# Optimization experiments

Hardware: AMD Instinct MI355X
Metric: run time of the kernel (lower is better)

## Reference

```python
import jax, jax.numpy as jnp
import numpy as np

RADIUS = 0.4
NSAMPLE = 32


def setup_inputs() -> dict:
    key = jax.random.key(0)
    ks = jax.random.split(key, 6)
    B, N, C = 2, 16384, 64
    xyz = jax.random.normal(ks[0], (B, N, 3), jnp.float32)
    features = jax.random.normal(ks[1], (B, C, N), jnp.float32)

    def w(k, i, o):
        return jax.random.normal(k, (i, o), jnp.float32) * (1.0 / np.sqrt(i))

    W1 = w(ks[2], C + 3, 64)
    W2 = w(ks[3], 64, 64)
    W3 = w(ks[4], 64, 128)
    return {
        "xyz": xyz, "features": features,
        "W1": W1, "b1": jnp.zeros((64,), jnp.float32),
        "W2": W2, "b2": jnp.zeros((64,), jnp.float32),
        "W3": W3, "b3": jnp.zeros((128,), jnp.float32),
        "npoint": 4096,
    }


def ball_query(xyz, new_xyz, radius, nsample):
    """xyz [B,N,3], new_xyz [B,S,3] -> neighbor idx [B,S,nsample] int32.
    Replicates pointnet2 ball_query: first `nsample` points (in index order)
    within `radius` of each centroid; empty slots filled with the first hit
    (0 if no point is in range)."""
    N = xyz.shape[1]
    # squared distances [B,S,N] via ||a||^2 + ||b||^2 - 2 a.b
    d2 = (jnp.sum(new_xyz * new_xyz, -1)[:, :, None]
          + jnp.sum(xyz * xyz, -1)[:, None, :]
          - 2.0 * jnp.einsum('bsc,bnc->bsn', new_xyz, xyz))
    cand = jnp.where(d2 < radius * radius,
                     jnp.arange(N, dtype=jnp.int32), jnp.int32(N))
    neg_topk, _ = jax.lax.top_k(-cand, nsample)  # nsample smallest indices
    idx = -neg_topk
    first = idx[..., :1]
    idx = jnp.where(idx == N, first, idx)  # pad with first valid neighbor
    idx = jnp.where(idx == N, 0, idx)      # no neighbor at all -> 0
    return idx


def reference(xyz, features, W1, b1, W2, b2, W3, b3, npoint):
    B = xyz.shape[0]
    # sample_method=None, keep_first_half=False -> idx = arange(npoint)
    new_xyz = xyz[:, :npoint]                        # [B,S,3]
    idx = ball_query(jax.lax.stop_gradient(xyz),
                     jax.lax.stop_gradient(new_xyz), RADIUS, NSAMPLE)
    # group: gather neighbors, re-center xyz, concat features (use_xyz=True)
    grouped_xyz = jax.vmap(lambda p, i: p[i])(xyz, idx) - new_xyz[:, :, None]  # [B,S,K,3]
    feats_nc = features.transpose(0, 2, 1)           # [B,N,C]
    grouped_f = jax.vmap(lambda f, i: f[i])(feats_nc, idx)  # [B,S,K,C]
    g = jnp.concatenate([grouped_xyz, grouped_f], axis=-1)  # [B,S,K,3+C]
    # shared MLP (1x1 convs + ReLU)
    h = jax.nn.relu(jnp.einsum('bskc,cd->bskd', g, W1) + b1)
    h = jax.nn.relu(jnp.einsum('bskc,cd->bskd', h, W2) + b2)
    h = jax.nn.relu(jnp.einsum('bskc,cd->bskd', h, W3) + b3)
    new_features = jnp.max(h, axis=2).transpose(0, 2, 1)    # [B,128,S]
    samp_idx = jnp.tile(jnp.arange(npoint, dtype=jnp.int32), (B, 1))
    return new_xyz, new_features, samp_idx
```

## Files before the change

kernel.cpp:

```cpp
#include <hip/hip_runtime.h>

#define BB 2
#define NN 16384
#define CC 64
#define SS 4096
#define KK 32
#define R2 0.16f

#define GD   32
#define GC   (GD * GD * GD)
#define CAP  1024
#define CAPL (CAP / 64)

typedef __bf16 bf16x8 __attribute__((ext_vector_type(8)));
typedef float  f32x4  __attribute__((ext_vector_type(4)));

#define MFMA(a, b, c) __builtin_amdgcn_mfma_f32_16x16x32_bf16((a), (b), (c), 0, 0, 0)

static __device__ __forceinline__ ushort f2bf(float f) {
    __bf16 h = (__bf16)f;
    return *(ushort*)&h;
}

static __device__ __forceinline__ int cellc(float x) {
    int i = (int)floorf(x * 2.5f + 16.0f);
    return i < 0 ? 0 : (i > GD - 1 ? GD - 1 : i);
}

#define WS_PTS4   0
#define WS_FEAT   524288
#define WS_W1T    4718592
#define WS_W2T    4730880
#define WS_W3T    4739072
#define WS_SPTS   4755456
#define WS_SSID   5279744
#define WS_CNT    5410816
#define WS_OFF    5672960

#define T_PTS   (BB * NN)
#define T_W1    (T_PTS + 64 * 96)
#define T_W2    (T_W1 + 64 * 64)
#define T_W3    (T_W2 + 128 * 64)
#define T_NXYZ  (T_W3 + BB * SS * 3)
#define T_SIDX  (T_NXYZ + BB * SS)
#define T_ALL   (T_SIDX + BB * NN * 8)

__global__ __launch_bounds__(256) void prep_kernel(
        const float* __restrict__ xyz, const float* __restrict__ feat,
        const float* __restrict__ W1, const float* __restrict__ W2,
        const float* __restrict__ W3,
        float4* __restrict__ pts4, ushort* __restrict__ feat_nc,
        ushort* __restrict__ W1t, ushort* __restrict__ W2t,
        ushort* __restrict__ W3t,
        float* __restrict__ out_xyz, float* __restrict__ out_sidx,
        uint* __restrict__ counts) {
    const int t = blockIdx.x * 256 + threadIdx.x;
    if (t < T_PTS) {
        const float* p = xyz + (size_t)t * 3;
        const float x = p[0], y = p[1], z = p[2];
        pts4[t] = make_float4(x, y, z, x * x + y * y + z * z);
        const int cell = (((cellc(z) << 5) + cellc(y)) << 5) + cellc(x);
        atomicAdd(&counts[(t >> 14) * GC + cell], 1u);
    } else if (t < T_W1) {
        const int i = t - T_PTS;
        const int n = i / 96, k = i - n * 96;
        float v = 0.0f;
        if (k < 64) v = W1[(3 + k) * 64 + n];
        else if (k < 67) v = W1[(k - 64) * 64 + n];
        W1t[n * 96 + k] = f2bf(v);
    } else if (t < T_W2) {
        const int i = t - T_W1;
        const int n = i >> 6, k = i & 63;
        W2t[n * 64 + k] = f2bf(W2[k * 64 + n]);
    } else if (t < T_W3) {
        const int i = t - T_W2;
        const int n = i >> 6, k = i & 63;
        W3t[n * 64 + k] = f2bf(W3[k * 128 + n]);
    } else if (t < T_NXYZ) {
        const int i = t - T_W3;
        const int b = i / (SS * 3), j = i - b * (SS * 3);
        out_xyz[i] = xyz[(size_t)b * NN * 3 + j];
    } else if (t < T_SIDX) {
        const int i = t - T_NXYZ;
        out_sidx[i] = (float)(i & (SS - 1));
    } else if (t < T_ALL) {
        const int j = t - T_SIDX;
        const int nl = j >> 3, c8 = j & 7;
        const int b = nl >> 14, n = nl & (NN - 1);
        const float* fb = feat + (size_t)b * CC * NN + n;
        uint u[4];
        #pragma unroll
        for (int q = 0; q < 4; ++q) {
            const float f0 = fb[(size_t)(c8 * 8 + 2 * q) * NN];
            const float f1 = fb[(size_t)(c8 * 8 + 2 * q + 1) * NN];
            u[q] = (uint)f2bf(f0) | ((uint)f2bf(f1) << 16);
        }
        *(uint4*)(feat_nc + (size_t)nl * 64 + c8 * 8) = make_uint4(u[0], u[1], u[2], u[3]);
    }
}

__global__ __launch_bounds__(1024) void scan_kernel(uint* __restrict__ counts,
                                                    uint* __restrict__ offs) {
    __shared__ int lds[1024];
    const int b = blockIdx.x, t = threadIdx.x;
    uint* cnts = counts + (size_t)b * GC;
    uint* off  = offs + (size_t)b * 32772;
    int sum = 0;
    #pragma unroll
    for (int j = 0; j < 8; ++j) {
        const uint4 v = *((const uint4*)cnts + t * 8 + j);
        sum += (int)(v.x + v.y + v.z + v.w);
    }
    lds[t] = sum;
    __syncthreads();
    for (int d = 1; d < 1024; d <<= 1) {
        const int add = (t >= d) ? lds[t - d] : 0;
        __syncthreads();
        lds[t] += add;
        __syncthreads();
    }
    int run = lds[t] - sum;
    #pragma unroll 4
    for (int j = 0; j < 32; ++j) {
        const int ci = t * 32 + j;
        const uint cv = cnts[ci];
        off[ci] = (uint)run;
        cnts[ci] = (uint)run;
        run += (int)cv;
    }
    if (t == 1023) off[GC] = (uint)run;
}

__global__ __launch_bounds__(256) void scatter_kernel(
        const float4* __restrict__ pts4, uint* __restrict__ counts,
        float4* __restrict__ spts, int* __restrict__ ssid) {
    const int t = blockIdx.x * 256 + threadIdx.x;
    const int b = t >> 14;
    const float4 p = pts4[t];
    const int cell = (((cellc(p.z) << 5) + cellc(p.y)) << 5) + cellc(p.x);
    const uint pos = atomicAdd(&counts[(size_t)b * GC + cell], 1u);
    spts[(size_t)b * NN + pos] = p;
    ssid[(size_t)b * NN + pos] = t & (NN - 1);
}

__global__ __launch_bounds__(256, 2) void fused_kernel(
        const float4* __restrict__ pts4, const ushort* __restrict__ feat_nc,
        const float4* __restrict__ spts, const int* __restrict__ ssid,
        const uint* __restrict__ offs,
        const ushort* __restrict__ W1t, const ushort* __restrict__ W2t,
        const ushort* __restrict__ W3t,
        const float* __restrict__ b1, const float* __restrict__ b2,
        const float* __restrict__ b3, float* __restrict__ out_feat) {
    const int w = threadIdx.x >> 6, lane = threadIdx.x & 63;
    const int quad = lane >> 4, mrow = lane & 15;
    const int m = lane & 31, half = lane >> 5;

    __shared__ __align__(16) ushort ldsA[4][32 * 104];
    __shared__ float stage[128][5];
    ushort* gbuf = ldsA[w];
    int* hit = (int*)gbuf;

    const int xcd = blockIdx.x & 7;
    const int slot = blockIdx.x >> 3;
    const int b = xcd >> 2;
    const int s0 = ((xcd & 3) * 256 + slot) * 4;
    const int s = s0 + w;

    const float4* pb = pts4 + (size_t)b * NN;
    const ushort* fbase = feat_nc + (size_t)b * NN * 64;
    const unsigned long long ltmask = (1ull << lane) - 1ull;

    {
        const float4 c = pb[s];
        const int cx = cellc(c.x), cy = cellc(c.y), cz = cellc(c.z);
        const int x0 = cx - 1 < 0 ? 0 : cx - 1;
        const int x1 = cx + 1 > GD - 1 ? GD - 1 : cx + 1;
        const uint* off = offs + (size_t)b * 32772;
        const float4* sp = spts + (size_t)b * NN;
        const int* sidp = ssid + (size_t)b * NN;
        int cnt = 0;
        #pragma unroll
        for (int e = 0; e < 9; ++e) {
            const int z = cz + e / 3 - 1, y = cy + e % 3 - 1;
            const bool ok = (z >= 0) && (z < GD) && (y >= 0) && (y < GD);
            const int cb = ((z << 5) + y) << 5;
            const int rs = ok ? (int)off[cb + x0] : 0;
            const int re = ok ? (int)off[cb + x1 + 1] : 0;
            for (int i0 = rs; i0 < re; i0 += 64) {
                const int iw = i0 + lane;
                const int ii = iw < re - 1 ? iw : re - 1;
                const bool act = iw < re;
                const float4 p = sp[ii];
                const int id = sidp[ii];
                const float d = c.w + p.w - 2.0f * (c.x * p.x + c.y * p.y + c.z * p.z);
                const bool h = act && (d < R2);
                const unsigned long long mk = __ballot(h);
                if (mk != 0ull) {
                    if (h) {
                        const int pp = cnt + __popcll(mk & ltmask);
                        if (pp < CAP) hit[pp] = id;
                    }
                    cnt += __popcll(mk);
                }
            }
        }
        if (cnt > KK) {
            const int stored = cnt < CAP ? cnt : CAP;
            int v[CAPL];
            #pragma unroll
            for (int j = 0; j < CAPL; ++j) {
                const int q = j * 64 + lane;
                v[j] = (q < stored) ? hit[q] : 0x7fffffff;
            }
            int lo = 0, hi = NN - 1;
            while (lo < hi) {
                const int mid = (lo + hi) >> 1;
                int cle = 0;
                #pragma unroll
                for (int j = 0; j < CAPL; ++j) cle += (v[j] <= mid) ? 1 : 0;
                #pragma unroll
                for (int o = 1; o < 64; o <<= 1) cle += __shfl_xor(cle, o);
                if (cle >= KK) hi = mid; else lo = mid + 1;
            }
            int pos = 0;
            #pragma unroll
            for (int j = 0; j < CAPL; ++j) {
                const bool sel = v[j] <= lo;
                const unsigned long long mk = __ballot(sel);
                if (sel) hit[pos + __popcll(mk & ltmask)] = v[j];
                pos += __popcll(mk);
            }
        } else if (lane < KK) {
            const int vv = (cnt == 0) ? 0 : ((lane < cnt) ? hit[lane] : hit[0]);
            hit[lane] = vv;
        }
    }

    {
        const int sid = hit[m];
        const ushort* src = fbase + (size_t)sid * 64 + half * 32;
        ushort* dst = gbuf + m * 104 + half * 32;
        uint4 rows[4];
        #pragma unroll
        for (int i = 0; i < 4; ++i) rows[i] = *(const uint4*)(src + i * 8);
        const float4 p = pb[sid];
        const float4 cc = pb[s];
        #pragma unroll
        for (int i = 0; i < 4; ++i) *(uint4*)(dst + i * 8) = rows[i];
        if (half == 0) {
            bf16x8 rel = {(__bf16)(p.x - cc.x), (__bf16)(p.y - cc.y),
                          (__bf16)(p.z - cc.z), (__bf16)0.f,
                          (__bf16)0.f, (__bf16)0.f, (__bf16)0.f, (__bf16)0.f};
            *(bf16x8*)(gbuf + m * 104 + 64) = rel;
            *(uint4*)(gbuf + m * 104 + 88) = make_uint4(0, 0, 0, 0);
        } else {
            *(uint4*)(gbuf + m * 104 + 72) = make_uint4(0, 0, 0, 0);
            *(uint4*)(gbuf + m * 104 + 80) = make_uint4(0, 0, 0, 0);
        }
    }

    {
        f32x4 acc[2][4];
        #pragma unroll
        for (int nt = 0; nt < 4; ++nt) {
            const float bv = b1[nt * 16 + mrow];
            acc[0][nt] = (f32x4){bv, bv, bv, bv};
            acc[1][nt] = acc[0][nt];
        }
        #pragma unroll
        for (int ks = 0; ks < 3; ++ks) {
            const bf16x8 a0 = *(const bf16x8*)(gbuf + mrow * 104 + ks * 32 + quad * 8);
            const bf16x8 a1 = *(const bf16x8*)(gbuf + (16 + mrow) * 104 + ks * 32 + quad * 8);
            #pragma unroll
            for (int nt = 0; nt < 4; ++nt) {
                const bf16x8 wf = *(const bf16x8*)(W1t + (nt * 16 + mrow) * 96 + ks * 32 + quad * 8);
                acc[0][nt] = MFMA(a0, wf, acc[0][nt]);
                acc[1][nt] = MFMA(a1, wf, acc[1][nt]);
            }
        }
        #pragma unroll
        for (int mt = 0; mt < 2; ++mt)
            #pragma unroll
            for (int nt = 0; nt < 4; ++nt)
                #pragma unroll
                for (int r = 0; r < 4; ++r)
                    gbuf[(mt * 16 + quad * 4 + r) * 104 + nt * 16 + mrow] =
                        f2bf(fmaxf(acc[mt][nt][r], 0.0f));
    }

    {
        f32x4 acc[2][4];
        #pragma unroll
        for (int nt = 0; nt < 4; ++nt) {
            const float bv = b2[nt * 16 + mrow];
            acc[0][nt] = (f32x4){bv, bv, bv, bv};
            acc[1][nt] = acc[0][nt];
        }
        #pragma unroll
        for (int ks = 0; ks < 2; ++ks) {
            const bf16x8 a0 = *(const bf16x8*)(gbuf + mrow * 104 + ks * 32 + quad * 8);
            const bf16x8 a1 = *(const bf16x8*)(gbuf + (16 + mrow) * 104 + ks * 32 + quad * 8);
            #pragma unroll
            for (int nt = 0; nt < 4; ++nt) {
                const bf16x8 wf = *(const bf16x8*)(W2t + (nt * 16 + mrow) * 64 + ks * 32 + quad * 8);
                acc[0][nt] = MFMA(a0, wf, acc[0][nt]);
                acc[1][nt] = MFMA(a1, wf, acc[1][nt]);
            }
        }
        #pragma unroll
        for (int mt = 0; mt < 2; ++mt)
            #pragma unroll
            for (int nt = 0; nt < 4; ++nt)
                #pragma unroll
                for (int r = 0; r < 4; ++r)
                    gbuf[(mt * 16 + quad * 4 + r) * 104 + nt * 16 + mrow] =
                        f2bf(fmaxf(acc[mt][nt][r], 0.0f));
    }

    #pragma unroll
    for (int nh = 0; nh < 2; ++nh) {
        f32x4 acc[2][4];
        #pragma unroll
        for (int ntl = 0; ntl < 4; ++ntl) {
            const float bv = b3[(nh * 4 + ntl) * 16 + mrow];
            acc[0][ntl] = (f32x4){bv, bv, bv, bv};
            acc[1][ntl] = acc[0][ntl];
        }
        #pragma unroll
        for (int ks = 0; ks < 2; ++ks) {
            const bf16x8 a0 = *(const bf16x8*)(gbuf + mrow * 104 + ks * 32 + quad * 8);
            const bf16x8 a1 = *(const bf16x8*)(gbuf + (16 + mrow) * 104 + ks * 32 + quad * 8);
            #pragma unroll
            for (int ntl = 0; ntl < 4; ++ntl) {
                const bf16x8 wf = *(const bf16x8*)(
                    W3t + ((nh * 4 + ntl) * 16 + mrow) * 64 + ks * 32 + quad * 8);
                acc[0][ntl] = MFMA(a0, wf, acc[0][ntl]);
                acc[1][ntl] = MFMA(a1, wf, acc[1][ntl]);
            }
        }
        #pragma unroll
        for (int ntl = 0; ntl < 4; ++ntl) {
            const f32x4 v0 = acc[0][ntl], v1 = acc[1][ntl];
            float mx = fmaxf(fmaxf(v0[0], v0[1]), fmaxf(v0[2], v0[3]));
            mx = fmaxf(mx, fmaxf(fmaxf(v1[0], v1[1]), fmaxf(v1[2], v1[3])));
            mx = fmaxf(mx, __shfl_xor(mx, 16));
            mx = fmaxf(mx, __shfl_xor(mx, 32));
            mx = fmaxf(mx, 0.0f);
            if (quad == 0) stage[(nh * 4 + ntl) * 16 + mrow][w] = mx;
        }
    }
    __syncthreads();

    {
        const int ch = threadIdx.x & 127;
        const int hf = threadIdx.x >> 7;
        float* dst = out_feat + ((size_t)b * 128 + ch) * SS + s0 + hf * 2;
        *(float2*)dst = make_float2(stage[ch][hf * 2], stage[ch][hf * 2 + 1]);
    }
}

extern "C" void kernel_launch(void* const* d_in, const int* in_sizes, int n_in,
                              void* d_out, int out_size, void* d_ws, size_t ws_size,
                              hipStream_t stream) {
    const float* xyz  = (const float*)d_in[0];
    const float* feat = (const float*)d_in[1];
    const float* W1   = (const float*)d_in[2];
    const float* b1   = (const float*)d_in[3];
    const float* W2   = (const float*)d_in[4];
    const float* b2   = (const float*)d_in[5];
    const float* W3   = (const float*)d_in[6];
    const float* b3   = (const float*)d_in[7];

    float* out      = (float*)d_out;
    float* out_xyz  = out;
    float* out_feat = out + (size_t)BB * SS * 3;
    float* out_sidx = out_feat + (size_t)BB * 128 * SS;

    char* ws = (char*)d_ws;
    float4* pts4    = (float4*)(ws + WS_PTS4);
    ushort* feat_nc = (ushort*)(ws + WS_FEAT);
    ushort* W1t     = (ushort*)(ws + WS_W1T);
    ushort* W2t     = (ushort*)(ws + WS_W2T);
    ushort* W3t     = (ushort*)(ws + WS_W3T);
    float4* spts    = (float4*)(ws + WS_SPTS);
    int*    ssid    = (int*)(ws + WS_SSID);
    uint*   counts  = (uint*)(ws + WS_CNT);
    uint*   offs    = (uint*)(ws + WS_OFF);

    hipMemsetAsync(counts, 0, (size_t)BB * GC * 4, stream);
    prep_kernel<<<(T_ALL + 255) / 256, 256, 0, stream>>>(
        xyz, feat, W1, W2, W3, pts4, feat_nc, W1t, W2t, W3t, out_xyz, out_sidx,
        counts);
    scan_kernel<<<BB, 1024, 0, stream>>>(counts, offs);
    scatter_kernel<<<BB * NN / 256, 256, 0, stream>>>(pts4, counts, spts, ssid);
    fused_kernel<<<BB * SS / 4, 256, 0, stream>>>(pts4, feat_nc, spts, ssid, offs,
                                                  W1t, W2t, W3t, b1, b2, b3,
                                                  out_feat);
}
```

Measured before the change: 168.3 us.

## Shrink grid, fuse histogram/scan/scatter into one LDS bin kernel, flatten neighbor scan

The uniform grid shrinks from 32^3 to 24^3 cells so its histogram fits in LDS. The memset, scan and scatter launches are replaced by one per-batch kernel that builds the histogram with LDS atomics, does a wave-shuffle scan and scatters points. Prep now writes only per-point cell ids. In the fused kernel, the nine candidate ranges are merged into one flat loop so partial wave iterations are shared across ranges, and the hit cap is halved with ballot-based counting in the selection step. The bin kernel runs on only two blocks, which may serialize, and the smaller cap could overflow in dense regions.

```diff
diff --git a/kernel.cpp b/kernel.cpp
--- a/kernel.cpp
+++ b/kernel.cpp
@@ -7,9 +7,10 @@
 #define KK 32
 #define R2 0.16f
 
-#define GD   32
+#define GD   24
 #define GC   (GD * GD * GD)
-#define CAP  1024
+#define GCP  (GC + 4)
+#define CAP  512
 #define CAPL (CAP / 64)
 
 typedef __bf16 bf16x8 __attribute__((ext_vector_type(8)));
@@ -23,7 +24,7 @@
 }
 
 static __device__ __forceinline__ int cellc(float x) {
-    int i = (int)floorf(x * 2.5f + 16.0f);
+    int i = (int)floorf(x * 2.5f + 12.0f);
     return i < 0 ? 0 : (i > GD - 1 ? GD - 1 : i);
 }
 
@@ -34,8 +35,8 @@
 #define WS_W3T    4739072
 #define WS_SPTS   4755456
 #define WS_SSID   5279744
-#define WS_CNT    5410816
-#define WS_OFF    5672960
+#define WS_CELLS  5410816
+#define WS_OFF    5476352
 
 #define T_PTS   (BB * NN)
 #define T_W1    (T_PTS + 64 * 96)
@@ -53,14 +54,13 @@
         ushort* __restrict__ W1t, ushort* __restrict__ W2t,
         ushort* __restrict__ W3t,
         float* __restrict__ out_xyz, float* __restrict__ out_sidx,
-        uint* __restrict__ counts) {
+        ushort* __restrict__ cells) {
     const int t = blockIdx.x * 256 + threadIdx.x;
     if (t < T_PTS) {
         const float* p = xyz + (size_t)t * 3;
         const float x = p[0], y = p[1], z = p[2];
         pts4[t] = make_float4(x, y, z, x * x + y * y + z * z);
-        const int cell = (((cellc(z) << 5) + cellc(y)) << 5) + cellc(x);
-        atomicAdd(&counts[(t >> 14) * GC + cell], 1u);
+        cells[t] = (ushort)((cellc(z) * GD + cellc(y)) * GD + cellc(x));
     } else if (t < T_W1) {
         const int i = t - T_PTS;
         const int n = i / 96, k = i - n * 96;
@@ -99,48 +99,60 @@
     }
 }
 
-__global__ __launch_bounds__(1024) void scan_kernel(uint* __restrict__ counts,
-                                                    uint* __restrict__ offs) {
-    __shared__ int lds[1024];
+#define CH 14
+__global__ __launch_bounds__(1024) void bin_kernel(
+        const float4* __restrict__ pts4, const ushort* __restrict__ cells,
+        float4* __restrict__ spts, int* __restrict__ ssid,
+        uint* __restrict__ offs) {
+    __shared__ uint hist[GC];
+    __shared__ uint wsum[17];
     const int b = blockIdx.x, t = threadIdx.x;
-    uint* cnts = counts + (size_t)b * GC;
-    uint* off  = offs + (size_t)b * 32772;
-    int sum = 0;
+    const ushort* cb = cells + (size_t)b * NN;
+
+    for (int i = t; i < GC; i += 1024) hist[i] = 0u;
+    __syncthreads();
+    for (int i = t; i < NN; i += 1024) atomicAdd(&hist[cb[i]], 1u);
+    __syncthreads();
+
+    uint c[CH];
+    uint s = 0;
     #pragma unroll
-    for (int j = 0; j < 8; ++j) {
-        const uint4 v = *((const uint4*)cnts + t * 8 + j);
-        sum += (int)(v.x + v.y + v.z + v.w);
-    }
-    lds[t] = sum;
-    __syncthreads();
-    for (int d = 1; d < 1024; d <<= 1) {
-        const int add = (t >= d) ? lds[t - d] : 0;
-        __syncthreads();
-        lds[t] += add;
-        __syncthreads();
-    }
-    int run = lds[t] - sum;
-    #pragma unroll 4
-    for (int j = 0; j < 32; ++j) {
-        const int ci = t * 32 + j;
-        const uint cv = cnts[ci];
-        off[ci] = (uint)run;
-        cnts[ci] = (uint)run;
-        run += (int)cv;
-    }
-    if (t == 1023) off[GC] = (uint)run;
-}
-
-__global__ __launch_bounds__(256) void scatter_kernel(
-        const float4* __restrict__ pts4, uint* __restrict__ counts,
-        float4* __restrict__ spts, int* __restrict__ ssid) {
-    const int t = blockIdx.x * 256 + threadIdx.x;
-    const int b = t >> 14;
-    const float4 p = pts4[t];
-    const int cell = (((cellc(p.z) << 5) + cellc(p.y)) << 5) + cellc(p.x);
-    const uint pos = atomicAdd(&counts[(size_t)b * GC + cell], 1u);
-    spts[(size_t)b * NN + pos] = p;
-    ssid[(size_t)b * NN + pos] = t & (NN - 1);
+    for (int j = 0; j < CH; ++j) {
+        const int ci = t * CH + j;
+        c[j] = (ci < GC) ? hist[ci] : 0u;
+        s += c[j];
+    }
+    const int lane = t & 63, wid = t >> 6;
+    uint inc = s;
+    #pragma unroll
+    for (int o = 1; o < 64; o <<= 1) {
+        const uint u = __shfl_up(inc, o);
+        inc += (lane >= o) ? u : 0u;
+    }
+    if (lane == 63) wsum[wid] = inc;
+    __syncthreads();
+    if (t == 0) {
+        uint r = 0;
+        #pragma unroll
+        for (int k = 0; k < 16; ++k) { const uint v2 = wsum[k]; wsum[k] = r; r += v2; }
+    }
+    __syncthreads();
+    uint run = wsum[wid] + inc - s;
+    uint* offb = offs + (size_t)b * GCP;
+    #pragma unroll
+    for (int j = 0; j < CH; ++j) {
+        const int ci = t * CH + j;
+        if (ci < GC) { offb[ci] = run; hist[ci] = run; run += c[j]; }
+    }
+    if (t == 1023) offb[GC] = NN;
+    __syncthreads();
+
+    for (int i = t; i < NN; i += 1024) {
+        const int cell = cb[i];
+        const uint pos = atomicAdd(&hist[cell], 1u);
+        spts[(size_t)b * NN + pos] = pts4[(size_t)b * NN + i];
+        ssid[(size_t)b * NN + pos] = i;
+    }
 }
 
 __global__ __launch_bounds__(256, 2) void fused_kernel(
@@ -175,60 +187,73 @@
         const int cx = cellc(c.x), cy = cellc(c.y), cz = cellc(c.z);
         const int x0 = cx - 1 < 0 ? 0 : cx - 1;
         const int x1 = cx + 1 > GD - 1 ? GD - 1 : cx + 1;
-        const uint* off = offs + (size_t)b * 32772;
+        const uint* off = offs + (size_t)b * GCP;
         const float4* sp = spts + (size_t)b * NN;
         const int* sidp = ssid + (size_t)b * NN;
-        int cnt = 0;
+
+        int rs[9], re[9], pre[10];
+        pre[0] = 0;
         #pragma unroll
         for (int e = 0; e < 9; ++e) {
             const int z = cz + e / 3 - 1, y = cy + e % 3 - 1;
             const bool ok = (z >= 0) && (z < GD) && (y >= 0) && (y < GD);
-            const int cb = ((z << 5) + y) << 5;
-            const int rs = ok ? (int)off[cb + x0] : 0;
-            const int re = ok ? (int)off[cb + x1 + 1] : 0;
-            for (int i0 = rs; i0 < re; i0 += 64) {
-                const int iw = i0 + lane;
-                const int ii = iw < re - 1 ? iw : re - 1;
-                const bool act = iw < re;
-                const float4 p = sp[ii];
-                const int id = sidp[ii];
-                const float d = c.w + p.w - 2.0f * (c.x * p.x + c.y * p.y + c.z * p.z);
-                const bool h = act && (d < R2);
-                const unsigned long long mk = __ballot(h);
-                if (mk != 0ull) {
-                    if (h) {
-                        const int pp = cnt + __popcll(mk & ltmask);
-                        if (pp < CAP) hit[pp] = id;
-                    }
-                    cnt += __popcll(mk);
-                }
-            }
-        }
+            const int cbase = (z * GD + y) * GD;
+            const int a = ok ? (int)off[cbase + x0] : 0;
+            const int bnd = ok ? (int)off[cbase + x1 + 1] : 0;
+            rs[e] = a;
+            re[e] = ok ? bnd : a;
+            pre[e + 1] = pre[e] + (re[e] - rs[e]);
+        }
+        const int tot = pre[9];
+
+        int cnt = 0;
+        for (int g0 = 0; g0 < tot; g0 += 64) {
+            const int g = g0 + lane;
+            int adj = rs[0];
+            #pragma unroll
+            for (int k = 1; k < 9; ++k) adj = (g >= pre[k]) ? (rs[k] - pre[k]) : adj;
+            const bool act = g < tot;
+            const int idx = act ? (g + adj) : 0;
+            const float4 p = sp[idx];
+            const int id = sidp[idx];
+            const float d = c.w + p.w - 2.0f * (c.x * p.x + c.y * p.y + c.z * p.z);
+            const bool h = act && (d < R2);
+            const unsigned long long mk = __ballot(h);
+            if (h) {
+                const int pp = cnt + __popcll(mk & ltmask);
+                if (pp < CAP) hit[pp] = id;
+            }
+            cnt += (int)__popcll(mk);
+        }
+
         if (cnt > KK) {
             const int stored = cnt < CAP ? cnt : CAP;
             int v[CAPL];
             #pragma unroll
             for (int j = 0; j < CAPL; ++j) {
                 const int q = j * 64 + lane;
-                v[j] = (q < stored) ? hit[q] : 0x7fffffff;
+                const int val = hit[q];
+                v[j] = (q < stored) ? val : 0x7fffffff;
             }
             int lo = 0, hi = NN - 1;
             while (lo < hi) {
                 const int mid = (lo + hi) >> 1;
                 int cle = 0;
                 #pragma unroll
-                for (int j = 0; j < CAPL; ++j) cle += (v[j] <= mid) ? 1 : 0;
-                #pragma unroll
-                for (int o = 1; o < 64; o <<= 1) cle += __shfl_xor(cle, o);
+                for (int j = 0; j < CAPL; ++j)
+                    if (j * 64 < stored)
+                        cle += (int)__popcll(__ballot(v[j] <= mid));
                 if (cle >= KK) hi = mid; else lo = mid + 1;
             }
             int pos = 0;
             #pragma unroll
             for (int j = 0; j < CAPL; ++j) {
-                const bool sel = v[j] <= lo;
-                const unsigned long long mk = __ballot(sel);
-                if (sel) hit[pos + __popcll(mk & ltmask)] = v[j];
-                pos += __popcll(mk);
+                if (j * 64 < stored) {
+                    const bool sel = v[j] <= lo;
+                    const unsigned long long mk = __ballot(sel);
+                    if (sel) hit[pos + __popcll(mk & ltmask)] = v[j];
+                    pos += (int)__popcll(mk);
+                }
             }
         } else if (lane < KK) {
             const int vv = (cnt == 0) ? 0 : ((lane < cnt) ? hit[lane] : hit[0]);
@@ -384,15 +409,13 @@
     ushort* W3t     = (ushort*)(ws + WS_W3T);
     float4* spts    = (float4*)(ws + WS_SPTS);
     int*    ssid    = (int*)(ws + WS_SSID);
-    uint*   counts  = (uint*)(ws + WS_CNT);
+    ushort* cells   = (ushort*)(ws + WS_CELLS);
     uint*   offs    = (uint*)(ws + WS_OFF);
 
-    hipMemsetAsync(counts, 0, (size_t)BB * GC * 4, stream);
     prep_kernel<<<(T_ALL + 255) / 256, 256, 0, stream>>>(
         xyz, feat, W1, W2, W3, pts4, feat_nc, W1t, W2t, W3t, out_xyz, out_sidx,
-        counts);
-    scan_kernel<<<BB, 1024, 0, stream>>>(counts, offs);
-    scatter_kernel<<<BB * NN / 256, 256, 0, stream>>>(pts4, counts, spts, ssid);
+        cells);
+    bin_kernel<<<BB, 1024, 0, stream>>>(pts4, cells, spts, ssid, offs);
     fused_kernel<<<BB * SS / 4, 256, 0, stream>>>(pts4, feat_nc, spts, ssid, offs,
                                                   W1t, W2t, W3t, b1, b2, b3,
                                                   out_feat);
```

After: 172.2 us. 2.3% more time.
